# Kernel optimization log

Measured on AMD Instinct MI355X. Metric: run time of the kernel, lower is better.

## Reference

```python
import jax, jax.numpy as jnp
import numpy as np

# Module hyperparameters (from init_kwargs)
K = 3          # kernel size
STRIDE = 1
PAD = 1
DIL = 1
DG = 1         # deformable groups
GROUPS = 1     # conv groups


def setup_inputs() -> dict:
    key = jax.random.key(0)
    k1, k2, k3, k4 = jax.random.split(key, 4)
    inputs = jax.random.normal(k1, (8, 64, 96, 96), dtype=jnp.float32)
    offset = jax.random.normal(k2, (8, DG * 2 * K * K, 96, 96), dtype=jnp.float32)
    mask = jax.random.uniform(k3, (8, DG * K * K, 96, 96), dtype=jnp.float32)
    # xavier-ish scale for the conv weight
    weight = jax.random.normal(k4, (64, 64, K, K), dtype=jnp.float32) * 0.05
    return {"inputs": inputs, "offset": offset, "mask": mask, "weight": weight}


def _bilinear_sample(xg, py, px):
    """xg: [N, dg, Cg, H, W]; py, px: [N, dg, P] fractional coords.
    Out-of-bounds samples contribute zero (DCN convention)."""
    N, dg, Cg, H, W = xg.shape
    xf = xg.reshape(N, dg, Cg, H * W)
    y0 = jnp.floor(py)
    x0 = jnp.floor(px)
    wy1 = py - y0
    wx1 = px - x0
    wy0 = 1.0 - wy1
    wx0 = 1.0 - wx1
    y0i = y0.astype(jnp.int32)
    x0i = x0.astype(jnp.int32)
    y1i = y0i + 1
    x1i = x0i + 1

    def gather(yi, xi, w):
        valid = (yi >= 0) & (yi < H) & (xi >= 0) & (xi < W)
        idx = jnp.clip(yi, 0, H - 1) * W + jnp.clip(xi, 0, W - 1)  # [N,dg,P]
        idx_b = jnp.broadcast_to(idx[:, :, None, :], (N, dg, Cg, idx.shape[-1]))
        v = jnp.take_along_axis(xf, idx_b, axis=-1)  # [N,dg,Cg,P]
        return v * (w * valid)[:, :, None, :]

    return (gather(y0i, x0i, wy0 * wx0) + gather(y0i, x1i, wy0 * wx1)
            + gather(y1i, x0i, wy1 * wx0) + gather(y1i, x1i, wy1 * wx1))


def reference(inputs, offset, mask, weight):
    N, C, H, W = inputs.shape
    Cout = weight.shape[0]
    KK = K * K
    Hout = (H + 2 * PAD - DIL * (K - 1) - 1) // STRIDE + 1
    Wout = (W + 2 * PAD - DIL * (K - 1) - 1) // STRIDE + 1

    # offset channels: per deformable group, per kernel tap, (dy, dx) interleaved
    off = offset.reshape(N, DG, KK, 2, Hout, Wout)
    m = mask.reshape(N, DG, KK, Hout, Wout)

    ky, kx = jnp.meshgrid(jnp.arange(K), jnp.arange(K), indexing="ij")
    ky = ky.reshape(KK).astype(jnp.float32)
    kx = kx.reshape(KK).astype(jnp.float32)
    gy = (jnp.arange(Hout) * STRIDE - PAD).astype(jnp.float32)
    gx = (jnp.arange(Wout) * STRIDE - PAD).astype(jnp.float32)
    base_y = ky[:, None, None] * DIL + gy[None, :, None]  # [KK,Hout,1]
    base_x = kx[:, None, None] * DIL + gx[None, None, :]  # [KK,1,Wout]

    py = off[:, :, :, 0] + base_y  # [N,DG,KK,Hout,Wout]
    px = off[:, :, :, 1] + base_x

    P = KK * Hout * Wout
    xg = inputs.reshape(N, DG, C // DG, H, W)
    sampled = _bilinear_sample(xg, py.reshape(N, DG, P), px.reshape(N, DG, P))
    sampled = sampled.reshape(N, DG, C // DG, KK, Hout, Wout) * m[:, :, None]
    cols = sampled.reshape(N, C, KK, Hout, Wout)

    # groups == 1: single GEMM over (C, KK)
    out = jnp.einsum("nckhw,ock->nohw", cols, weight.reshape(Cout, C, KK))
    return out
```

## Files before the change

kernel.cpp:

```cpp
#include <hip/hip_runtime.h>

#define HWX 9216
#define CIN 64
#define COUT 64
#define SR 14
#define SC 24
#define SLOT 144

typedef __attribute__((ext_vector_type(8))) short short8;
typedef __attribute__((ext_vector_type(8))) _Float16 half8;
typedef __attribute__((ext_vector_type(2))) _Float16 half2v;
typedef __attribute__((ext_vector_type(4))) float f32x4;
typedef __attribute__((ext_vector_type(4))) unsigned int u32x4;

__device__ inline unsigned short f2h(float f) {
    union { _Float16 h; unsigned short u; } v;
    v.h = (_Float16)f;
    return v.u;
}
__device__ inline unsigned pack2h(float lo, float hi) {
    return (unsigned)f2h(lo) | ((unsigned)f2h(hi) << 16);
}

__global__ __launch_bounds__(256) void dcn_pre(const float* __restrict__ x,
                                               unsigned* __restrict__ xt,
                                               const float* __restrict__ w,
                                               unsigned short* __restrict__ wA) {
    if (blockIdx.x < 1152) {
        __shared__ float tile[64][65];
        int n  = blockIdx.x / 144;
        int p0 = (blockIdx.x % 144) * 64;
        const float* xp = x + (size_t)n * CIN * HWX + p0;
        #pragma unroll
        for (int it = 0; it < 16; ++it) {
            int px = threadIdx.x & 63;
            int c  = (threadIdx.x >> 6) + it * 4;
            tile[c][px] = xp[c * HWX + px];
        }
        __syncthreads();
        unsigned* xo = xt + ((size_t)n * HWX + p0) * 32;
        #pragma unroll
        for (int it = 0; it < 8; ++it) {
            int c2 = threadIdx.x & 31;
            int px = (threadIdx.x >> 5) + it * 8;
            xo[px * 32 + c2] = pack2h(tile[2 * c2][px], tile[2 * c2 + 1][px]);
        }
    } else {
        int idx = (blockIdx.x - 1152) * 256 + threadIdx.x;
        int j    = idx & 7;
        int lane = (idx >> 3) & 63;
        int m0   = (idx >> 9) & 3;
        int step = idx >> 11;
        int co = m0 * 16 + (lane & 15);
        int kg = step * 32 + ((lane >> 4) << 3) + j;
        int kk = kg >> 6;
        int c  = kg & 63;
        wA[idx] = f2h(w[(co * 64 + c) * 9 + kk]);
    }
}

__global__ __launch_bounds__(384, 4) void dcn_fwd(const unsigned short* __restrict__ xt,
                                                  const float* __restrict__ offset,
                                                  const float* __restrict__ mask,
                                                  const unsigned short* __restrict__ wA,
                                                  float* __restrict__ out) {
    __shared__ __align__(16) char ldsx[SR * SC * SLOT];

    int bid = blockIdx.x;
    int swz = (bid & 7) * 96 + (bid >> 3);
    int n   = swz / 96;
    int t0  = swz % 96;
    int r0  = (t0 / 6) * 6;
    int c0  = (t0 % 6) * 16;

    int sy0 = r0 - 4;
    int sx0 = c0 - 4;

    const unsigned short* xn = xt + (size_t)n * HWX * 64;

    int wave = threadIdx.x >> 6;
    int lane = threadIdx.x & 63;
    int l15  = lane & 15;
    int lg   = lane >> 4;

    int ho = r0 + wave;
    int wo = c0 + l15;

    float dyv[9], dxv[9], mv[9];
    #pragma unroll
    for (int kk = 0; kk < 9; ++kk) {
        dyv[kk] = offset[((n * 18 + 2 * kk + 0) * 96 + ho) * 96 + wo];
        dxv[kk] = offset[((n * 18 + 2 * kk + 1) * 96 + ho) * 96 + wo];
        mv[kk]  = mask[((n * 9 + kk) * 96 + ho) * 96 + wo];
    }

    #pragma unroll
    for (int it = 0; it < 7; ++it) {
        int i  = threadIdx.x + it * 384;
        int s  = i >> 3, ch = i & 7;
        int ly = s / SC, lx = s - ly * SC;
        int gy = min(max(sy0 + ly, 0), 95);
        int gx = min(max(sx0 + lx, 0), 95);
        *(u32x4*)(ldsx + s * SLOT + ch * 16) =
            *((const u32x4*)(xn + (gy * 96 + gx) * 64) + ch);
    }
    __syncthreads();

    f32x4 acc[4] = {f32x4{0,0,0,0}, f32x4{0,0,0,0}, f32x4{0,0,0,0}, f32x4{0,0,0,0}};

    int oh0 = lg * 16;
    int oh1 = 64 + lg * 16;
    int ch0 = lg * 8;
    int ch1 = 32 + lg * 8;

    #pragma unroll
    for (int kk = 0; kk < 9; ++kk) {
        int ky = kk / 3, kx = kk % 3;
        float dy = dyv[kk];
        float dx = dxv[kk];
        float m  = mv[kk];

        float py = dy + (float)(ky + ho - 1);
        float px = dx + (float)(kx + wo - 1);
        float y0f = floorf(py), x0f = floorf(px);
        float wy1 = py - y0f,  wx1 = px - x0f;
        float wy0 = 1.f - wy1, wx0 = 1.f - wx1;
        int y0 = (int)y0f, x0 = (int)x0f;
        int y1 = y0 + 1,   x1 = x0 + 1;
        bool vy0 = (y0 >= 0) && (y0 < 96);
        bool vy1 = (y1 >= 0) && (y1 < 96);
        bool vx0 = (x0 >= 0) && (x0 < 96);
        bool vx1 = (x1 >= 0) && (x1 < 96);
        int y0c = min(max(y0, 0), 95), y1c = min(max(y1, 0), 95);
        int x0c = min(max(x0, 0), 95), x1c = min(max(x1, 0), 95);
        float w00 = wy0 * wx0 * m * ((vy0 && vx0) ? 1.f : 0.f);
        float w01 = wy0 * wx1 * m * ((vy0 && vx1) ? 1.f : 0.f);
        float w10 = wy1 * wx0 * m * ((vy1 && vx0) ? 1.f : 0.f);
        float w11 = wy1 * wx1 * m * ((vy1 && vx1) ? 1.f : 0.f);

        _Float16 h00 = (_Float16)w00, h01 = (_Float16)w01;
        _Float16 h10 = (_Float16)w10, h11 = (_Float16)w11;
        half2v W00 = {h00, h00}, W01 = {h01, h01}, W10 = {h10, h10}, W11 = {h11, h11};

        bool local = (y0c >= sy0) & (y1c <= sy0 + SR - 1) &
                     (x0c >= sx0) & (x1c <= sx0 + SC - 1);
        int ly0 = min(max(y0c - sy0, 0), SR - 1);
        int ly1 = min(max(y1c - sy0, 0), SR - 1);
        int lx0 = min(max(x0c - sx0, 0), SC - 1);
        int lx1 = min(max(x1c - sx0, 0), SC - 1);
        int s00 = (ly0 * SC + lx0) * SLOT;
        int s01 = (ly0 * SC + lx1) * SLOT;
        int s10 = (ly1 * SC + lx0) * SLOT;
        int s11 = (ly1 * SC + lx1) * SLOT;

        union { u32x4 u; half2v h[4]; } a00, a01, a10, a11, b00, b01, b10, b11, rA, rB;
        a00.u = *(const u32x4*)(ldsx + s00 + oh0);
        a01.u = *(const u32x4*)(ldsx + s01 + oh0);
        a10.u = *(const u32x4*)(ldsx + s10 + oh0);
        a11.u = *(const u32x4*)(ldsx + s11 + oh0);
        b00.u = *(const u32x4*)(ldsx + s00 + oh1);
        b01.u = *(const u32x4*)(ldsx + s01 + oh1);
        b10.u = *(const u32x4*)(ldsx + s10 + oh1);
        b11.u = *(const u32x4*)(ldsx + s11 + oh1);

        if (__builtin_expect(!local, 0)) {
            int g00 = (y0c * 96 + x0c) * 64;
            int g01 = (y0c * 96 + x1c) * 64;
            int g10 = (y1c * 96 + x0c) * 64;
            int g11 = (y1c * 96 + x1c) * 64;
            a00.u = *(const u32x4*)(xn + g00 + ch0);
            a01.u = *(const u32x4*)(xn + g01 + ch0);
            a10.u = *(const u32x4*)(xn + g10 + ch0);
            a11.u = *(const u32x4*)(xn + g11 + ch0);
            b00.u = *(const u32x4*)(xn + g00 + ch1);
            b01.u = *(const u32x4*)(xn + g01 + ch1);
            b10.u = *(const u32x4*)(xn + g10 + ch1);
            b11.u = *(const u32x4*)(xn + g11 + ch1);
        }

        #pragma unroll
        for (int p = 0; p < 4; ++p) {
            rA.h[p] = a00.h[p] * W00 + a01.h[p] * W01 + a10.h[p] * W10 + a11.h[p] * W11;
            rB.h[p] = b00.h[p] * W00 + b01.h[p] * W01 + b10.h[p] * W10 + b11.h[p] * W11;
        }
        half8 bfragA = *(half8*)&rA;
        half8 bfragB = *(half8*)&rB;

        {
            int step = kk * 2;
            const half8* wp = (const half8*)(wA + (step * 256 + lane) * 8);
            acc[0] = __builtin_amdgcn_mfma_f32_16x16x32_f16(wp[0],   bfragA, acc[0], 0, 0, 0);
            acc[1] = __builtin_amdgcn_mfma_f32_16x16x32_f16(wp[64],  bfragA, acc[1], 0, 0, 0);
            acc[2] = __builtin_amdgcn_mfma_f32_16x16x32_f16(wp[128], bfragA, acc[2], 0, 0, 0);
            acc[3] = __builtin_amdgcn_mfma_f32_16x16x32_f16(wp[192], bfragA, acc[3], 0, 0, 0);
        }
        {
            int step = kk * 2 + 1;
            const half8* wp = (const half8*)(wA + (step * 256 + lane) * 8);
            acc[0] = __builtin_amdgcn_mfma_f32_16x16x32_f16(wp[0],   bfragB, acc[0], 0, 0, 0);
            acc[1] = __builtin_amdgcn_mfma_f32_16x16x32_f16(wp[64],  bfragB, acc[1], 0, 0, 0);
            acc[2] = __builtin_amdgcn_mfma_f32_16x16x32_f16(wp[128], bfragB, acc[2], 0, 0, 0);
            acc[3] = __builtin_amdgcn_mfma_f32_16x16x32_f16(wp[192], bfragB, acc[3], 0, 0, 0);
        }
    }

    size_t obase = (size_t)n * COUT * HWX + (size_t)ho * 96 + wo;
    #pragma unroll
    for (int m0 = 0; m0 < 4; ++m0) {
        #pragma unroll
        for (int r = 0; r < 4; ++r) {
            int co = m0 * 16 + lg * 4 + r;
            out[obase + (size_t)co * HWX] = acc[m0][r];
        }
    }
}

extern "C" void kernel_launch(void* const* d_in, const int* in_sizes, int n_in,
                              void* d_out, int out_size, void* d_ws, size_t ws_size,
                              hipStream_t stream) {
    const float* x      = (const float*)d_in[0];
    const float* offset = (const float*)d_in[1];
    const float* mask   = (const float*)d_in[2];
    const float* w      = (const float*)d_in[3];
    float* out = (float*)d_out;
    unsigned* xt       = (unsigned*)d_ws;
    unsigned short* wA = (unsigned short*)((char*)d_ws + (size_t)8 * HWX * 64 * 2);

    hipLaunchKernelGGL(dcn_pre, dim3(1296), dim3(256), 0, stream, x, xt, w, wA);
    hipLaunchKernelGGL(dcn_fwd, dim3(768), dim3(384), 0, stream,
                       (const unsigned short*)xt, offset, mask, wA, out);
}
```

Before: 31.03 us.

## Move non-local bilinear fallback out of main loop as wave-uniform correction pass

The main tap loop now always samples from the LDS tile, so the per-lane divergent global-load branch no longer sits inside it. Lanes whose samples fall outside the tile are recorded in per-lane and wave-wide bitmasks. A second pass runs only for taps where some lane in the wave tripped. It recomputes the bilinear weights, forms the difference between the global-memory sample and the LDS sample, and adds that difference through extra MFMAs. This keeps the common path free of divergent branches, but it recomputes coordinates and issues extra MFMAs and loads for taps where any lane tripped, and the fp16 subtraction can add rounding error.

```diff
diff --git a/kernel.cpp b/kernel.cpp
--- a/kernel.cpp
+++ b/kernel.cpp
@@ -108,20 +108,19 @@
 
     f32x4 acc[4] = {f32x4{0,0,0,0}, f32x4{0,0,0,0}, f32x4{0,0,0,0}, f32x4{0,0,0,0}};
 
-    int oh0 = lg * 16;
-    int oh1 = 64 + lg * 16;
-    int ch0 = lg * 8;
-    int ch1 = 32 + lg * 8;
+    const int oh0 = lg * 16;
+    const int oh1 = 64 + lg * 16;
+    const int ch0 = lg * 8;
+    const int ch1 = 32 + lg * 8;
+
+    unsigned laneMask = 0;
+    unsigned anyMask  = 0;
 
     #pragma unroll
     for (int kk = 0; kk < 9; ++kk) {
-        int ky = kk / 3, kx = kk % 3;
-        float dy = dyv[kk];
-        float dx = dxv[kk];
+        float py = dyv[kk] + (float)(kk / 3 + ho - 1);
+        float px = dxv[kk] + (float)(kk % 3 + wo - 1);
         float m  = mv[kk];
-
-        float py = dy + (float)(ky + ho - 1);
-        float px = dx + (float)(kx + wo - 1);
         float y0f = floorf(py), x0f = floorf(px);
         float wy1 = py - y0f,  wx1 = px - x0f;
         float wy0 = 1.f - wy1, wx0 = 1.f - wx1;
@@ -144,6 +143,9 @@
 
         bool local = (y0c >= sy0) & (y1c <= sy0 + SR - 1) &
                      (x0c >= sx0) & (x1c <= sx0 + SC - 1);
+        laneMask |= (local ? 0u : 1u) << kk;
+        if (__any(!local)) anyMask |= 1u << kk;
+
         int ly0 = min(max(y0c - sy0, 0), SR - 1);
         int ly1 = min(max(y1c - sy0, 0), SR - 1);
         int lx0 = min(max(x0c - sx0, 0), SC - 1);
@@ -163,44 +165,98 @@
         b10.u = *(const u32x4*)(ldsx + s10 + oh1);
         b11.u = *(const u32x4*)(ldsx + s11 + oh1);
 
-        if (__builtin_expect(!local, 0)) {
+        #pragma unroll
+        for (int p = 0; p < 4; ++p) {
+            rA.h[p] = a00.h[p] * W00 + a01.h[p] * W01 + a10.h[p] * W10 + a11.h[p] * W11;
+            rB.h[p] = b00.h[p] * W00 + b01.h[p] * W01 + b10.h[p] * W10 + b11.h[p] * W11;
+        }
+        half8 bfragA = *(half8*)&rA;
+        half8 bfragB = *(half8*)&rB;
+
+        {
+            const half8* wp = (const half8*)(wA + ((kk * 2) * 256 + lane) * 8);
+            acc[0] = __builtin_amdgcn_mfma_f32_16x16x32_f16(wp[0],   bfragA, acc[0], 0, 0, 0);
+            acc[1] = __builtin_amdgcn_mfma_f32_16x16x32_f16(wp[64],  bfragA, acc[1], 0, 0, 0);
+            acc[2] = __builtin_amdgcn_mfma_f32_16x16x32_f16(wp[128], bfragA, acc[2], 0, 0, 0);
+            acc[3] = __builtin_amdgcn_mfma_f32_16x16x32_f16(wp[192], bfragA, acc[3], 0, 0, 0);
+        }
+        {
+            const half8* wp = (const half8*)(wA + ((kk * 2 + 1) * 256 + lane) * 8);
+            acc[0] = __builtin_amdgcn_mfma_f32_16x16x32_f16(wp[0],   bfragB, acc[0], 0, 0, 0);
+            acc[1] = __builtin_amdgcn_mfma_f32_16x16x32_f16(wp[64],  bfragB, acc[1], 0, 0, 0);
+            acc[2] = __builtin_amdgcn_mfma_f32_16x16x32_f16(wp[128], bfragB, acc[2], 0, 0, 0);
+            acc[3] = __builtin_amdgcn_mfma_f32_16x16x32_f16(wp[192], bfragB, acc[3], 0, 0, 0);
+        }
+    }
+
+    #pragma unroll
+    for (int kk = 0; kk < 9; ++kk) {
+        if (anyMask & (1u << kk)) {
+            bool tripped = (laneMask >> kk) & 1u;
+            float py = dyv[kk] + (float)(kk / 3 + ho - 1);
+            float px = dxv[kk] + (float)(kk % 3 + wo - 1);
+            float m  = mv[kk];
+            float y0f = floorf(py), x0f = floorf(px);
+            float wy1 = py - y0f,  wx1 = px - x0f;
+            float wy0 = 1.f - wy1, wx0 = 1.f - wx1;
+            int y0 = (int)y0f, x0 = (int)x0f;
+            int y1 = y0 + 1,   x1 = x0 + 1;
+            bool vy0 = (y0 >= 0) && (y0 < 96);
+            bool vy1 = (y1 >= 0) && (y1 < 96);
+            bool vx0 = (x0 >= 0) && (x0 < 96);
+            bool vx1 = (x1 >= 0) && (x1 < 96);
+            int y0c = min(max(y0, 0), 95), y1c = min(max(y1, 0), 95);
+            int x0c = min(max(x0, 0), 95), x1c = min(max(x1, 0), 95);
+            float w00 = wy0 * wx0 * m * ((vy0 && vx0) ? 1.f : 0.f);
+            float w01 = wy0 * wx1 * m * ((vy0 && vx1) ? 1.f : 0.f);
+            float w10 = wy1 * wx0 * m * ((vy1 && vx0) ? 1.f : 0.f);
+            float w11 = wy1 * wx1 * m * ((vy1 && vx1) ? 1.f : 0.f);
+            _Float16 h00 = (_Float16)w00, h01 = (_Float16)w01;
+            _Float16 h10 = (_Float16)w10, h11 = (_Float16)w11;
+            half2v W00 = {h00, h00}, W01 = {h01, h01}, W10 = {h10, h10}, W11 = {h11, h11};
+
+            int ly0 = min(max(y0c - sy0, 0), SR - 1);
+            int ly1 = min(max(y1c - sy0, 0), SR - 1);
+            int lx0 = min(max(x0c - sx0, 0), SC - 1);
+            int lx1 = min(max(x1c - sx0, 0), SC - 1);
+            int s00 = (ly0 * SC + lx0) * SLOT;
+            int s01 = (ly0 * SC + lx1) * SLOT;
+            int s10 = (ly1 * SC + lx0) * SLOT;
+            int s11 = (ly1 * SC + lx1) * SLOT;
             int g00 = (y0c * 96 + x0c) * 64;
             int g01 = (y0c * 96 + x1c) * 64;
             int g10 = (y1c * 96 + x0c) * 64;
             int g11 = (y1c * 96 + x1c) * 64;
-            a00.u = *(const u32x4*)(xn + g00 + ch0);
-            a01.u = *(const u32x4*)(xn + g01 + ch0);
-            a10.u = *(const u32x4*)(xn + g10 + ch0);
-            a11.u = *(const u32x4*)(xn + g11 + ch0);
-            b00.u = *(const u32x4*)(xn + g00 + ch1);
-            b01.u = *(const u32x4*)(xn + g01 + ch1);
-            b10.u = *(const u32x4*)(xn + g10 + ch1);
-            b11.u = *(const u32x4*)(xn + g11 + ch1);
-        }
-
-        #pragma unroll
-        for (int p = 0; p < 4; ++p) {
-            rA.h[p] = a00.h[p] * W00 + a01.h[p] * W01 + a10.h[p] * W10 + a11.h[p] * W11;
-            rB.h[p] = b00.h[p] * W00 + b01.h[p] * W01 + b10.h[p] * W10 + b11.h[p] * W11;
-        }
-        half8 bfragA = *(half8*)&rA;
-        half8 bfragB = *(half8*)&rB;
-
-        {
-            int step = kk * 2;
-            const half8* wp = (const half8*)(wA + (step * 256 + lane) * 8);
-            acc[0] = __builtin_amdgcn_mfma_f32_16x16x32_f16(wp[0],   bfragA, acc[0], 0, 0, 0);
-            acc[1] = __builtin_amdgcn_mfma_f32_16x16x32_f16(wp[64],  bfragA, acc[1], 0, 0, 0);
-            acc[2] = __builtin_amdgcn_mfma_f32_16x16x32_f16(wp[128], bfragA, acc[2], 0, 0, 0);
-            acc[3] = __builtin_amdgcn_mfma_f32_16x16x32_f16(wp[192], bfragA, acc[3], 0, 0, 0);
-        }
-        {
-            int step = kk * 2 + 1;
-            const half8* wp = (const half8*)(wA + (step * 256 + lane) * 8);
-            acc[0] = __builtin_amdgcn_mfma_f32_16x16x32_f16(wp[0],   bfragB, acc[0], 0, 0, 0);
-            acc[1] = __builtin_amdgcn_mfma_f32_16x16x32_f16(wp[64],  bfragB, acc[1], 0, 0, 0);
-            acc[2] = __builtin_amdgcn_mfma_f32_16x16x32_f16(wp[128], bfragB, acc[2], 0, 0, 0);
-            acc[3] = __builtin_amdgcn_mfma_f32_16x16x32_f16(wp[192], bfragB, acc[3], 0, 0, 0);
+
+            half2v z = {(_Float16)0.f, (_Float16)0.f};
+
+            #pragma unroll
+            for (int half = 0; half < 2; ++half) {
+                const int oh = half ? oh1 : oh0;
+                const int ch = half ? ch1 : ch0;
+                union { u32x4 u; half2v h[4]; } t00, t01, t10, t11, q00, q01, q10, q11, rT, rW;
+                t00.u = *(const u32x4*)(xn + g00 + ch);
+                t01.u = *(const u32x4*)(xn + g01 + ch);
+                t10.u = *(const u32x4*)(xn + g10 + ch);
+                t11.u = *(const u32x4*)(xn + g11 + ch);
+                q00.u = *(const u32x4*)(ldsx + s00 + oh);
+                q01.u = *(const u32x4*)(ldsx + s01 + oh);
+                q10.u = *(const u32x4*)(ldsx + s10 + oh);
+                q11.u = *(const u32x4*)(ldsx + s11 + oh);
+                #pragma unroll
+                for (int p = 0; p < 4; ++p) {
+                    half2v tb = t00.h[p] * W00 + t01.h[p] * W01 + t10.h[p] * W10 + t11.h[p] * W11;
+                    half2v wb = q00.h[p] * W00 + q01.h[p] * W01 + q10.h[p] * W10 + q11.h[p] * W11;
+                    half2v d  = tb - wb;
+                    rT.h[p] = tripped ? d : z;
+                }
+                half8 dfrag = *(half8*)&rT;
+                const half8* wp = (const half8*)(wA + ((kk * 2 + half) * 256 + lane) * 8);
+                acc[0] = __builtin_amdgcn_mfma_f32_16x16x32_f16(wp[0],   dfrag, acc[0], 0, 0, 0);
+                acc[1] = __builtin_amdgcn_mfma_f32_16x16x32_f16(wp[64],  dfrag, acc[1], 0, 0, 0);
+                acc[2] = __builtin_amdgcn_mfma_f32_16x16x32_f16(wp[128], dfrag, acc[2], 0, 0, 0);
+                acc[3] = __builtin_amdgcn_mfma_f32_16x16x32_f16(wp[192], dfrag, acc[3], 0, 0, 0);
+            }
         }
     }
 
```

After: 64.50 us. 2.08x slower.
